# Optimization experiments

Measured on AMD Instinct MI355X. Metric: run time of the kernel, lower is better.

## Reference

```python
import jax, jax.numpy as jnp
import numpy as np

N_NODES = 50000
IN_CH = 128
OUT_CH = 64
N_EDGES = 800000


def setup_inputs() -> dict:
    key = jax.random.key(0)
    k_x, k_e, k_w, k_b = jax.random.split(key, 4)
    x = jax.random.normal(k_x, (N_NODES, IN_CH), dtype=jnp.float32)
    edge_index = jax.random.randint(k_e, (2, N_EDGES), 0, N_NODES, dtype=jnp.int64)
    # nn.Linear(in, out, bias=False): weight [out, in], applied as x @ W^T
    W = jax.random.normal(k_w, (OUT_CH, IN_CH), dtype=jnp.float32) * (1.0 / np.sqrt(IN_CH))
    bias = jax.random.normal(k_b, (OUT_CH,), dtype=jnp.float32) * 0.02
    return {"x": x, "edge_index": edge_index, "W": W, "bias": bias}


def reference(x, edge_index, W, bias):
    # linear projection (no bias): [N, in] @ [in, out] -> [N, out]
    h = x @ W.T
    src = edge_index[0]
    dst = edge_index[1]
    # gather source node feats per edge: [E, out]
    msgs = h[src]
    # scatter_add into dest nodes: [N, out]
    out = jax.ops.segment_sum(msgs, dst, num_segments=h.shape[0])
    return out + bias
```

## Files before the change

kernel.cpp:

```cpp
#include <hip/hip_runtime.h>

#define IN_CH 128
#define OUT_CH 64
#define TN 64
#define XS_STRIDE 132
#define WS_STRIDE 129

#define PBLOCKS 512
#define NB 800
#define CAPA 8
#define DCAP 32
#define OCAP 64

__device__ __forceinline__ unsigned f2bf(float f) {
    unsigned u = __float_as_uint(f);
    return (u + 0x7FFFu + ((u >> 16) & 1u)) >> 16;
}

__device__ __forceinline__ void fma4(float4& acc, float s, const float4& wv) {
    acc.x += s * wv.x;
    acc.y += s * wv.y;
    acc.z += s * wv.z;
    acc.w += s * wv.w;
}

__global__ __launch_bounds__(256) void k_fusedA(const float* __restrict__ x,
                                                const float* __restrict__ W,
                                                unsigned* __restrict__ h16,
                                                const int* __restrict__ ei,
                                                unsigned* __restrict__ cells,
                                                uint2* __restrict__ spill,
                                                int* __restrict__ spillCount,
                                                int nNodes, int nEdges, int totalBlocks) {
    __shared__ float smem[TN * XS_STRIDE + IN_CH * OUT_CH];
    __shared__ int is64s;
    int tid = threadIdx.x;

    int i = blockIdx.x;
    long long t = (long long)i * PBLOCKS;
    int pid = (int)(t / totalBlocks);
    int isPartA = (int)((t + PBLOCKS) / totalBlocks) > pid;

    if (isPartA) {
        unsigned* lists = (unsigned*)smem;
        int* curs = (int*)smem + NB * CAPA;
        for (int k = tid; k < NB; k += 256) curs[k] = 0;
        if (tid == 0) {
            int v = 1;
#pragma unroll
            for (int j = 0; j < 16; ++j)
                if (ei[2 * j + 1] != 0) v = 0;
            is64s = v;
        }
        __syncthreads();
        int is64 = is64s;

        int chunk = (nEdges + PBLOCKS - 1) / PBLOCKS;
        int e0 = pid * chunk;
        int e1 = min(e0 + chunk, nEdges);
        for (int e = e0 + tid; e < e1; e += 256) {
            int src, dst;
            if (is64) {
                src = ((const int2*)ei)[e].x;
                dst = ((const int2*)ei)[nEdges + e].x;
            } else {
                src = ei[e];
                dst = ei[nEdges + e];
            }
            if ((unsigned)src >= (unsigned)nNodes) src = 0;
            if ((unsigned)dst >= (unsigned)nNodes) dst = 0;
            int bucket = dst >> 6;
            int rank = (bucket < NB) ? atomicAdd(&curs[bucket], 1) : CAPA;
            if (rank < CAPA) {
                lists[bucket * CAPA + rank] = (unsigned)src | ((unsigned)(dst & 63) << 16);
            } else {
                int sp = atomicAdd(spillCount, 1);
                if (sp < nEdges) spill[sp] = make_uint2((unsigned)src, (unsigned)dst);
            }
        }
        __syncthreads();

        for (int cell = tid; cell < NB; cell += 256) {
            uint4 v0 = *(const uint4*)(lists + cell * CAPA);
            uint4 v1 = *(const uint4*)(lists + cell * CAPA + 4);
            v0.x = (v0.x & 0x0FFFFFFFu) | ((unsigned)min(curs[cell], CAPA) << 28);
            uint4* dst4 = (uint4*)(cells + ((size_t)cell * PBLOCKS + pid) * CAPA);
            dst4[0] = v0;
            dst4[1] = v1;
        }
        return;
    }

    int gid = i - pid;
    float* u  = smem;
    float* wt = smem + TN * XS_STRIDE;
    int nodeBase = gid * TN;

    {
        const float4* W4 = (const float4*)W;
        for (int j = tid; j < IN_CH * OUT_CH / 4; j += 256) {
            float4 v = W4[j];
            int o = j >> 5;
            int k = (j & 31) * 4;
            float* d = u + o * WS_STRIDE + k;
            d[0] = v.x; d[1] = v.y; d[2] = v.z; d[3] = v.w;
        }
    }
    __syncthreads();
    {
        int o = tid & 63;
        int k0 = (tid >> 6) * 32;
#pragma unroll 8
        for (int k = k0; k < k0 + 32; ++k)
            wt[k * OUT_CH + o] = u[o * WS_STRIDE + k];
    }
    __syncthreads();
    {
        int remRows = nNodes - nodeBase;
        if (remRows > TN) remRows = TN;
        const float4* X4 = (const float4*)(x + (size_t)nodeBase * IN_CH);
        for (int j = tid; j < TN * IN_CH / 4; j += 256) {
            int r = j >> 5;
            int k = (j & 31) * 4;
            float4 v = make_float4(0.f, 0.f, 0.f, 0.f);
            if (r < remRows) v = X4[j];
            *(float4*)(u + r * XS_STRIDE + k) = v;
        }
    }
    __syncthreads();

    int tx = tid & 15;
    int ty = tid >> 4;

    float4 acc[4];
#pragma unroll
    for (int q = 0; q < 4; ++q) acc[q] = make_float4(0.f, 0.f, 0.f, 0.f);

    const float* wcol = wt + tx * 4;
#pragma unroll 4
    for (int k = 0; k < IN_CH; k += 4) {
        float4 w0 = *(const float4*)(wcol + (k + 0) * OUT_CH);
        float4 w1 = *(const float4*)(wcol + (k + 1) * OUT_CH);
        float4 w2 = *(const float4*)(wcol + (k + 2) * OUT_CH);
        float4 w3 = *(const float4*)(wcol + (k + 3) * OUT_CH);
#pragma unroll
        for (int q = 0; q < 4; ++q) {
            float4 a = *(const float4*)(u + (ty * 4 + q) * XS_STRIDE + k);
            fma4(acc[q], a.x, w0);
            fma4(acc[q], a.y, w1);
            fma4(acc[q], a.z, w2);
            fma4(acc[q], a.w, w3);
        }
    }

#pragma unroll
    for (int q = 0; q < 4; ++q) {
        int n = nodeBase + ty * 4 + q;
        if (n < nNodes) {
            uint2 pk;
            pk.x = f2bf(acc[q].x) | (f2bf(acc[q].y) << 16);
            pk.y = f2bf(acc[q].z) | (f2bf(acc[q].w) << 16);
            *(uint2*)(h16 + (size_t)n * 32 + tx * 2) = pk;
        }
    }
}

__global__ __launch_bounds__(512, 8) void k_fusedB(const unsigned* __restrict__ cells,
                                                   const unsigned* __restrict__ h16,
                                                   const float* __restrict__ bias,
                                                   float* __restrict__ out,
                                                   const uint2* __restrict__ spill,
                                                   const int* __restrict__ spillCount,
                                                   int nNodes, int nEdges) {
    __shared__ unsigned nl[64 * DCAP];
    __shared__ int nc[64];
    __shared__ unsigned oS[OCAP];
    __shared__ int ocnt;
    int tid = threadIdx.x;
    int b = blockIdx.x;
    int nodeBase = b * 64;

    if (tid < 64) nc[tid] = 0;
    if (tid == 0) ocnt = 0;
    __syncthreads();

    if (b < NB) {
        for (int blk = tid; blk < PBLOCKS; blk += 512) {
            const unsigned* cb = cells + ((size_t)b * PBLOCKS + blk) * CAPA;
            uint4 w0 = *(const uint4*)(cb + 0);
            uint4 w1 = *(const uint4*)(cb + 4);
            int c = (int)(w0.x >> 28);
            if (c > CAPA) c = CAPA;
            unsigned w[CAPA] = {w0.x, w0.y, w0.z, w0.w, w1.x, w1.y, w1.z, w1.w};
#pragma unroll
            for (int r = 0; r < CAPA; ++r) {
                if (r < c) {
                    unsigned rec = w[r];
                    int sub = (int)(rec >> 16) & 63;
                    int rank = atomicAdd(&nc[sub], 1);
                    if (rank < DCAP) {
                        nl[sub * DCAP + rank] = rec & 0xFFFFu;
                    } else {
                        int rk = atomicAdd(&ocnt, 1);
                        if (rk < OCAP) oS[rk] = (rec & 0xFFFFu) | ((unsigned)sub << 16);
                    }
                }
            }
        }
    }

    {
        int sc = *spillCount;
        if (sc > nEdges) sc = nEdges;
        for (int e = tid; e < sc; e += 512) {
            uint2 sd = spill[e];
            if ((int)(sd.y >> 6) == b) {
                int sub = (int)(sd.y & 63);
                int rank = atomicAdd(&nc[sub], 1);
                if (rank < DCAP) {
                    nl[sub * DCAP + rank] = sd.x;
                } else {
                    int rk = atomicAdd(&ocnt, 1);
                    if (rk < OCAP) oS[rk] = sd.x | ((unsigned)sub << 16);
                }
            }
        }
    }
    __syncthreads();

    int lane = tid & 63;
    int wv   = tid >> 6;
    int q4   = lane >> 4;
    int cp   = lane & 15;
    float4 bv = *(const float4*)(bias + cp * 4);
    int oc = ocnt;
    if (oc > OCAP) oc = OCAP;

#pragma unroll
    for (int q = 0; q < 8; ++q) {
        int sub = wv * 8 + q;
        int node = nodeBase + sub;
        if (node >= nNodes) continue;

        int d = nc[sub];
        if (d > DCAP) d = DCAP;
        int base = sub * DCAP;

        float4 acc = {0.f, 0.f, 0.f, 0.f};
        for (int j = 0; j < d; j += 16) {
            int i0 = j + q4;
            int i1 = i0 + 4;
            int i2 = i0 + 8;
            int i3 = i0 + 12;
            int s0 = (int)nl[base + (i0 < d ? i0 : 0)];
            int s1 = (int)nl[base + (i1 < d ? i1 : 0)];
            int s2 = (int)nl[base + (i2 < d ? i2 : 0)];
            int s3 = (int)nl[base + (i3 < d ? i3 : 0)];
            uint2 v0 = *(const uint2*)(h16 + (size_t)s0 * 32 + cp * 2);
            uint2 v1 = *(const uint2*)(h16 + (size_t)s1 * 32 + cp * 2);
            uint2 v2 = *(const uint2*)(h16 + (size_t)s2 * 32 + cp * 2);
            uint2 v3 = *(const uint2*)(h16 + (size_t)s3 * 32 + cp * 2);
            if (i0 >= d) { v0.x = 0u; v0.y = 0u; }
            if (i1 >= d) { v1.x = 0u; v1.y = 0u; }
            if (i2 >= d) { v2.x = 0u; v2.y = 0u; }
            if (i3 >= d) { v3.x = 0u; v3.y = 0u; }
            acc.x += __uint_as_float(v0.x << 16);
            acc.y += __uint_as_float(v0.x & 0xFFFF0000u);
            acc.z += __uint_as_float(v0.y << 16);
            acc.w += __uint_as_float(v0.y & 0xFFFF0000u);
            acc.x += __uint_as_float(v1.x << 16);
            acc.y += __uint_as_float(v1.x & 0xFFFF0000u);
            acc.z += __uint_as_float(v1.y << 16);
            acc.w += __uint_as_float(v1.y & 0xFFFF0000u);
            acc.x += __uint_as_float(v2.x << 16);
            acc.y += __uint_as_float(v2.x & 0xFFFF0000u);
            acc.z += __uint_as_float(v2.y << 16);
            acc.w += __uint_as_float(v2.y & 0xFFFF0000u);
            acc.x += __uint_as_float(v3.x << 16);
            acc.y += __uint_as_float(v3.x & 0xFFFF0000u);
            acc.z += __uint_as_float(v3.y << 16);
            acc.w += __uint_as_float(v3.y & 0xFFFF0000u);
        }

        for (int t = 0; t < oc; ++t) {
            unsigned rec = oS[t];
            if ((int)(rec >> 16) == sub && q4 == 0) {
                int s = (int)(rec & 0xFFFFu);
                uint2 v = *(const uint2*)(h16 + (size_t)s * 32 + cp * 2);
                acc.x += __uint_as_float(v.x << 16);
                acc.y += __uint_as_float(v.x & 0xFFFF0000u);
                acc.z += __uint_as_float(v.y << 16);
                acc.w += __uint_as_float(v.y & 0xFFFF0000u);
            }
        }

        acc.x += __shfl_down(acc.x, 32, 64);
        acc.y += __shfl_down(acc.y, 32, 64);
        acc.z += __shfl_down(acc.z, 32, 64);
        acc.w += __shfl_down(acc.w, 32, 64);
        acc.x += __shfl_down(acc.x, 16, 64);
        acc.y += __shfl_down(acc.y, 16, 64);
        acc.z += __shfl_down(acc.z, 16, 64);
        acc.w += __shfl_down(acc.w, 16, 64);
        if (lane < 16) {
            float4 o;
            o.x = acc.x + bv.x;
            o.y = acc.y + bv.y;
            o.z = acc.z + bv.z;
            o.w = acc.w + bv.w;
            *(float4*)(out + (size_t)node * OUT_CH + cp * 4) = o;
        }
    }
}

extern "C" void kernel_launch(void* const* d_in, const int* in_sizes, int n_in,
                              void* d_out, int out_size, void* d_ws, size_t ws_size,
                              hipStream_t stream) {
    const float* x    = (const float*)d_in[0];
    const int*   ei   = (const int*)d_in[1];
    const float* W    = (const float*)d_in[2];
    const float* bias = (const float*)d_in[3];
    float* out = (float*)d_out;

    int nNodes = in_sizes[0] / IN_CH;
    int nEdges = in_sizes[1] / 2;
    int gemmBlocks = (nNodes + TN - 1) / TN;
    int realBuckets = (nNodes + 63) / 64;
    int totalBlocks = gemmBlocks + PBLOCKS;

    char* p = (char*)d_ws;
    auto alloc = [&](size_t bytes) {
        char* r = p;
        p += (bytes + 255) & ~(size_t)255;
        return r;
    };
    unsigned* h16        = (unsigned*)alloc((size_t)nNodes * 32 * sizeof(unsigned));
    unsigned* cells      = (unsigned*)alloc((size_t)PBLOCKS * NB * CAPA * sizeof(unsigned));
    uint2*    spill      = (uint2*)alloc((size_t)nEdges * sizeof(uint2));
    int*      spillCount = (int*)alloc(sizeof(int));

    hipMemsetAsync(spillCount, 0, sizeof(int), stream);
    k_fusedA<<<totalBlocks, 256, 0, stream>>>(x, W, h16, ei, cells,
                                              spill, spillCount, nNodes, nEdges, totalBlocks);
    k_fusedB<<<realBuckets, 512, 0, stream>>>(cells, h16, bias, out,
                                              spill, spillCount, nNodes, nEdges);
}
```

Before: 126.8 us.

## Restructure projection GEMM to one node row per thread with LDS weights

The GEMM part now assigns one node row to each thread. That thread reads its x row straight from global memory and accumulates all 64 outputs in registers, while the transposed W is kept in LDS and read as a broadcast. This drops the staging of x tiles in LDS, one barrier and the separate transpose pass. Blocks are also laid out with GEMM blocks first and edge-partition blocks after, instead of being interleaved by a division formula. In exchange, global loads and bf16 stores become strided per thread rather than coalesced, and there are far fewer GEMM blocks with higher register use per thread.

Result: slower. 135.9 us (+7.2%).

```diff
diff --git a/kernel.cpp b/kernel.cpp
--- a/kernel.cpp
+++ b/kernel.cpp
@@ -2,9 +2,8 @@
 
 #define IN_CH 128
 #define OUT_CH 64
-#define TN 64
-#define XS_STRIDE 132
-#define WS_STRIDE 129
+#define TN 256
+#define WT 68
 
 #define PBLOCKS 512
 #define NB 800
@@ -31,17 +30,14 @@
                                                 unsigned* __restrict__ cells,
                                                 uint2* __restrict__ spill,
                                                 int* __restrict__ spillCount,
-                                                int nNodes, int nEdges, int totalBlocks) {
-    __shared__ float smem[TN * XS_STRIDE + IN_CH * OUT_CH];
+                                                int nNodes, int nEdges, int gemmBlocks) {
+    __shared__ __align__(16) float smem[IN_CH * WT];
     __shared__ int is64s;
     int tid = threadIdx.x;
-
     int i = blockIdx.x;
-    long long t = (long long)i * PBLOCKS;
-    int pid = (int)(t / totalBlocks);
-    int isPartA = (int)((t + PBLOCKS) / totalBlocks) > pid;
-
-    if (isPartA) {
+
+    if (i >= gemmBlocks) {
+        int pid = i - gemmBlocks;
         unsigned* lists = (unsigned*)smem;
         int* curs = (int*)smem + NB * CAPA;
         for (int k = tid; k < NB; k += 256) curs[k] = 0;
@@ -91,76 +87,58 @@
         return;
     }
 
-    int gid = i - pid;
-    float* u  = smem;
-    float* wt = smem + TN * XS_STRIDE;
-    int nodeBase = gid * TN;
-
+    float* wt = smem;
     {
         const float4* W4 = (const float4*)W;
-        for (int j = tid; j < IN_CH * OUT_CH / 4; j += 256) {
-            float4 v = W4[j];
-            int o = j >> 5;
-            int k = (j & 31) * 4;
-            float* d = u + o * WS_STRIDE + k;
-            d[0] = v.x; d[1] = v.y; d[2] = v.z; d[3] = v.w;
+        for (int f = tid; f < IN_CH * OUT_CH / 4; f += 256) {
+            float4 v = W4[f];
+            int o  = f >> 5;
+            int k4 = (f & 31) * 4;
+            wt[(k4 + 0) * WT + o] = v.x;
+            wt[(k4 + 1) * WT + o] = v.y;
+            wt[(k4 + 2) * WT + o] = v.z;
+            wt[(k4 + 3) * WT + o] = v.w;
         }
     }
     __syncthreads();
-    {
-        int o = tid & 63;
-        int k0 = (tid >> 6) * 32;
-#pragma unroll 8
-        for (int k = k0; k < k0 + 32; ++k)
-            wt[k * OUT_CH + o] = u[o * WS_STRIDE + k];
-    }
-    __syncthreads();
-    {
-        int remRows = nNodes - nodeBase;
-        if (remRows > TN) remRows = TN;
-        const float4* X4 = (const float4*)(x + (size_t)nodeBase * IN_CH);
-        for (int j = tid; j < TN * IN_CH / 4; j += 256) {
-            int r = j >> 5;
-            int k = (j & 31) * 4;
-            float4 v = make_float4(0.f, 0.f, 0.f, 0.f);
-            if (r < remRows) v = X4[j];
-            *(float4*)(u + r * XS_STRIDE + k) = v;
-        }
-    }
-    __syncthreads();
-
-    int tx = tid & 15;
-    int ty = tid >> 4;
-
-    float4 acc[4];
-#pragma unroll
-    for (int q = 0; q < 4; ++q) acc[q] = make_float4(0.f, 0.f, 0.f, 0.f);
-
-    const float* wcol = wt + tx * 4;
-#pragma unroll 4
-    for (int k = 0; k < IN_CH; k += 4) {
-        float4 w0 = *(const float4*)(wcol + (k + 0) * OUT_CH);
-        float4 w1 = *(const float4*)(wcol + (k + 1) * OUT_CH);
-        float4 w2 = *(const float4*)(wcol + (k + 2) * OUT_CH);
-        float4 w3 = *(const float4*)(wcol + (k + 3) * OUT_CH);
-#pragma unroll
-        for (int q = 0; q < 4; ++q) {
-            float4 a = *(const float4*)(u + (ty * 4 + q) * XS_STRIDE + k);
-            fma4(acc[q], a.x, w0);
-            fma4(acc[q], a.y, w1);
-            fma4(acc[q], a.z, w2);
-            fma4(acc[q], a.w, w3);
-        }
-    }
-
-#pragma unroll
-    for (int q = 0; q < 4; ++q) {
-        int n = nodeBase + ty * 4 + q;
-        if (n < nNodes) {
+
+    int n = i * TN + tid;
+    bool act = n < nNodes;
+    const float4* xr = (const float4*)(x + (size_t)(act ? n : 0) * IN_CH);
+
+    float4 acc[16];
+#pragma unroll
+    for (int t = 0; t < 16; ++t) acc[t] = make_float4(0.f, 0.f, 0.f, 0.f);
+
+    for (int c = 0; c < 4; ++c) {
+        float4 xc[8];
+#pragma unroll
+        for (int r = 0; r < 8; ++r) xc[r] = xr[c * 8 + r];
+#pragma unroll
+        for (int k8 = 0; k8 < 8; ++k8) {
+            float4 xv = xc[k8];
+#pragma unroll
+            for (int kk = 0; kk < 4; ++kk) {
+                const float4* wr = (const float4*)(wt + (c * 32 + k8 * 4 + kk) * WT);
+                float s = (kk == 0) ? xv.x : (kk == 1) ? xv.y : (kk == 2) ? xv.z : xv.w;
+#pragma unroll
+                for (int t = 0; t < 16; ++t) fma4(acc[t], s, wr[t]);
+            }
+        }
+    }
+
+    if (act) {
+        unsigned* hp = h16 + (size_t)n * 32;
+#pragma unroll
+        for (int g = 0; g < 8; ++g) {
             uint2 pk;
-            pk.x = f2bf(acc[q].x) | (f2bf(acc[q].y) << 16);
-            pk.y = f2bf(acc[q].z) | (f2bf(acc[q].w) << 16);
-            *(uint2*)(h16 + (size_t)n * 32 + tx * 2) = pk;
+            pk.x = f2bf(acc[g * 2].x)     | (f2bf(acc[g * 2].y) << 16);
+            pk.y = f2bf(acc[g * 2].z)     | (f2bf(acc[g * 2].w) << 16);
+            *(uint2*)(hp + g * 4) = pk;
+            uint2 pk2;
+            pk2.x = f2bf(acc[g * 2 + 1].x) | (f2bf(acc[g * 2 + 1].y) << 16);
+            pk2.y = f2bf(acc[g * 2 + 1].z) | (f2bf(acc[g * 2 + 1].w) << 16);
+            *(uint2*)(hp + g * 4 + 2) = pk2;
         }
     }
 }
@@ -341,7 +319,7 @@
 
     hipMemsetAsync(spillCount, 0, sizeof(int), stream);
     k_fusedA<<<totalBlocks, 256, 0, stream>>>(x, W, h16, ei, cells,
-                                              spill, spillCount, nNodes, nEdges, totalBlocks);
+                                              spill, spillCount, nNodes, nEdges, gemmBlocks);
     k_fusedB<<<realBuckets, 512, 0, stream>>>(cells, h16, bias, out,
                                               spill, spillCount, nNodes, nEdges);
 }
```
